# Optimization experiments

Hardware: AMD Instinct MI355X
Metric: run time of the kernel (lower is better)

## Reference

```python
import jax, jax.numpy as jnp
import numpy as np


def setup_inputs() -> dict:
    key = jax.random.key(0)
    k1, k2, k3 = jax.random.split(key, 3)
    N, M, D = 8192, 32768, 64
    source_data = jax.random.normal(k1, (N, D), dtype=jnp.float32)
    target_data = jax.random.normal(k2, (M, D), dtype=jnp.float32)
    psi = jax.random.normal(k3, (M,), dtype=jnp.float32)
    return {"source_data": source_data, "target_data": target_data, "psi": psi}


def reference(source_data, target_data, psi):
    # cost[n, m] = ||x_n||^2 + ||y_m||^2 - 2 <x_n, y_m>
    sq_src = jnp.sum(source_data ** 2, axis=1, keepdims=True)          # [N, 1]
    sq_tgt = jnp.sum(target_data ** 2, axis=1)[None, :]                # [1, M]
    cost = sq_src + sq_tgt - 2.0 * jnp.einsum('nd,md->nm', source_data, target_data)
    out = jnp.min(cost - psi[None, :], axis=1) + jnp.mean(psi)         # [N]
    return out
```

## Files before the change

### kernel.cpp

```cpp
#include <hip/hip_runtime.h>
#include <stdint.h>

typedef float  f32x4v __attribute__((ext_vector_type(4)));
typedef short  s16x8  __attribute__((ext_vector_type(8)));

constexpr int D      = 64;
constexpr int SPLITS = 64;
constexpr int TILE_M = 128;
constexpr int G      = 16;
constexpr int NBUF   = 3;

__device__ __forceinline__ unsigned short f2bf(float f) {
    unsigned int u = __float_as_uint(f);
    u = (u + 0x7FFFu + ((u >> 16) & 1u)) >> 16;
    return (unsigned short)u;
}

__device__ __forceinline__ void gload_lds16(const void* g, void* l) {
    __builtin_amdgcn_global_load_lds((__attribute__((address_space(1))) void*)g,
                                     (__attribute__((address_space(3))) void*)l, 16, 0, 0);
}
__device__ __forceinline__ void gload_lds4(const void* g, void* l) {
    __builtin_amdgcn_global_load_lds((__attribute__((address_space(1))) void*)g,
                                     (__attribute__((address_space(3))) void*)l, 4, 0, 0);
}

__global__ __launch_bounds__(256)
void prep(const float* __restrict__ X, const float* __restrict__ Y,
          const float* __restrict__ psi,
          unsigned short* __restrict__ Xb, unsigned short* __restrict__ Yb,
          float* __restrict__ t, float* __restrict__ sqx,
          float* __restrict__ psum_arr, int N, int M) {
    const int tid  = threadIdx.x;
    const int lane = tid & 63, wave = tid >> 6;
    const int r16  = lane & 15, q = lane >> 4;
    const int NYB = M >> 4, NXB = N >> 4;
    const int b = blockIdx.x;
    __shared__ float red[4];

    if (b < NYB) {
        const int row = b * 16 + wave * 4 + q;
        const float4 v = *reinterpret_cast<const float4*>(Y + (size_t)row * D + r16 * 4);
        uint2 p;
        p.x = (unsigned)f2bf(v.x) | ((unsigned)f2bf(v.y) << 16);
        p.y = (unsigned)f2bf(v.z) | ((unsigned)f2bf(v.w) << 16);
        *reinterpret_cast<uint2*>(Yb + (size_t)row * D + r16 * 4) = p;
        float s = v.x * v.x + v.y * v.y + v.z * v.z + v.w * v.w;
        #pragma unroll
        for (int off = 1; off <= 8; off <<= 1) s += __shfl_xor(s, off);
        if (r16 == 0) t[row] = s - psi[row];
    } else if (b < NYB + NXB) {
        const int row = (b - NYB) * 16 + wave * 4 + q;
        const float4 v = *reinterpret_cast<const float4*>(X + (size_t)row * D + r16 * 4);
        uint2 p;
        p.x = (unsigned)f2bf(-2.f * v.x) | ((unsigned)f2bf(-2.f * v.y) << 16);
        p.y = (unsigned)f2bf(-2.f * v.z) | ((unsigned)f2bf(-2.f * v.w) << 16);
        *reinterpret_cast<uint2*>(Xb + (size_t)row * D + r16 * 4) = p;
        float s = v.x * v.x + v.y * v.y + v.z * v.z + v.w * v.w;
        #pragma unroll
        for (int off = 1; off <= 8; off <<= 1) s += __shfl_xor(s, off);
        if (r16 == 0) sqx[row] = s;
    } else {
        const int g = b - NYB - NXB;
        float s = psi[g * 512 + tid] + psi[g * 512 + 256 + tid];
        #pragma unroll
        for (int off = 1; off <= 32; off <<= 1) s += __shfl_xor(s, off);
        if (lane == 0) red[wave] = s;
        __syncthreads();
        if (tid == 0) psum_arr[g] = red[0] + red[1] + red[2] + red[3];
    }
}

__global__ __launch_bounds__(256, 2)
void sdot_main(const unsigned short* __restrict__ Xb,
               const unsigned short* __restrict__ Yb,
               const float* __restrict__ t,
               float* __restrict__ partial, int M) {
    __shared__ __align__(16) unsigned short ly[NBUF][TILE_M * D];
    __shared__ __align__(16) float lt[NBUF][256];

    const int tid  = threadIdx.x;
    const int wave = tid >> 6, lane = tid & 63;
    const int quad = lane >> 4, r16 = lane & 15;
    const int chunk  = blockIdx.x;
    const int rowgrp = blockIdx.y;
    const int CH      = M / SPLITS;
    const int m_begin = chunk * CH;
    const int NT      = CH / TILE_M;

    s16x8 b[G][2];
    #pragma unroll
    for (int g = 0; g < G; ++g) {
        const int srow = rowgrp * (G * 64) + wave * (G * 16) + g * 16 + r16;
        #pragma unroll
        for (int h = 0; h < 2; ++h)
            b[g][h] = *reinterpret_cast<const s16x8*>(Xb + (size_t)srow * D + h * 32 + quad * 8);
    }

    float rmin[G];
    #pragma unroll
    for (int g = 0; g < G; ++g) rmin[g] = 1e30f;

    auto stage = [&](int buf, int mb) {
        #pragma unroll
        for (int i = 0; i < 4; ++i) {
            const int idx = i * 256 + tid;
            const int row = idx >> 3, c = idx & 7;
            gload_lds16(Yb + (size_t)(mb + row) * D + ((c ^ (row & 7)) << 3),
                        &ly[buf][(i * 256 + wave * 64) << 3]);
        }
        gload_lds4(t + mb + wave * 64 + lane, &lt[buf][wave * 64]);
    };

    stage(0, m_begin);
    stage(1, m_begin + TILE_M);

    for (int tI = 0; tI < NT; ++tI) {
        if (tI < NT - 1) asm volatile("s_waitcnt vmcnt(5)" ::: "memory");
        else             asm volatile("s_waitcnt vmcnt(0)" ::: "memory");
        __builtin_amdgcn_s_barrier();
        if (tI + 2 < NT) stage((tI + 2) % NBUF, m_begin + (tI + 2) * TILE_M);
        const int buf = tI % NBUF;

        #pragma unroll
        for (int st = 0; st < TILE_M / 16; ++st) {
            const int trow = st * 16 + r16;
            const int sw   = trow & 7;
            const s16x8 a0 = *reinterpret_cast<const s16x8*>(
                                 &ly[buf][trow * D + ((quad ^ sw) << 3)]);
            const s16x8 a1 = *reinterpret_cast<const s16x8*>(
                                 &ly[buf][trow * D + (((quad + 4) ^ sw) << 3)]);
            const f32x4v tv4 = *reinterpret_cast<const f32x4v*>(
                                   &lt[buf][st * 16 + quad * 4]);
            #pragma unroll
            for (int g = 0; g < G; ++g) {
                f32x4v acc = __builtin_amdgcn_mfma_f32_16x16x32_bf16(a0, b[g][0], tv4, 0, 0, 0);
                acc        = __builtin_amdgcn_mfma_f32_16x16x32_bf16(a1, b[g][1], acc, 0, 0, 0);
                rmin[g] = fminf(fminf(fminf(acc[0], acc[1]), acc[2]),
                                fminf(acc[3], rmin[g]));
            }
        }
    }

    #pragma unroll
    for (int off = 16; off <= 32; off <<= 1)
        #pragma unroll
        for (int g = 0; g < G; ++g)
            rmin[g] = fminf(rmin[g], __shfl_xor(rmin[g], off));

    if (quad == 0) {
        #pragma unroll
        for (int g = 0; g < G; ++g) {
            const int row = rowgrp * (G * 64) + wave * (G * 16) + g * 16 + r16;
            partial[(size_t)row * SPLITS + chunk] = rmin[g];
        }
    }
}

__global__ __launch_bounds__(256)
void finalize(const float* __restrict__ sqx, const float* __restrict__ partial,
              const float* __restrict__ psum_arr, float* __restrict__ out, int M) {
    const int lane = threadIdx.x & 63, wave = threadIdx.x >> 6;
    const int row  = blockIdx.x * 4 + wave;
    float ps = psum_arr[lane];
    #pragma unroll
    for (int off = 1; off <= 32; off <<= 1) ps += __shfl_xor(ps, off);
    float pm = partial[(size_t)row * SPLITS + lane];
    #pragma unroll
    for (int off = 1; off <= 32; off <<= 1) pm = fminf(pm, __shfl_xor(pm, off));
    if (lane == 0) out[row] = sqx[row] + ps / (float)M + pm;
}

extern "C" void kernel_launch(void* const* d_in, const int* in_sizes, int n_in,
                              void* d_out, int out_size, void* d_ws, size_t ws_size,
                              hipStream_t stream) {
    const float* X   = (const float*)d_in[0];
    const float* Y   = (const float*)d_in[1];
    const float* psi = (const float*)d_in[2];
    float* out = (float*)d_out;

    const int N = in_sizes[0] / D;
    const int M = in_sizes[2];

    char* ws = (char*)d_ws;
    unsigned short* Yb = (unsigned short*)ws;
    size_t off = (size_t)M * D * sizeof(unsigned short);
    unsigned short* Xb = (unsigned short*)(ws + off);
    off += (size_t)N * D * sizeof(unsigned short);
    float* t = (float*)(ws + off);
    off += (size_t)M * sizeof(float);
    float* sqx = (float*)(ws + off);
    off += (size_t)N * sizeof(float);
    float* partial = (float*)(ws + off);
    off += (size_t)N * SPLITS * sizeof(float);
    float* psum_arr = (float*)(ws + off);

    prep<<<(M >> 4) + (N >> 4) + 64, 256, 0, stream>>>(X, Y, psi, Xb, Yb, t, sqx, psum_arr, N, M);
    sdot_main<<<dim3(SPLITS, N / 1024), 256, 0, stream>>>(Xb, Yb, t, partial, M);
    finalize<<<N / 4, 256, 0, stream>>>(sqx, partial, psum_arr, out, M);
}
```

Baseline: 100.6 us.

## Load whole chunk into LDS once and batch MFMAs with raised priority

Replaces the triple-buffered streaming of 128-row target tiles with a single bulk load of the block's full 512-row chunk into LDS, followed by one wait and barrier. The inner loop now issues all 16 first-half MFMAs, then all 16 second-half MFMAs, under s_setprio(1) before doing the min reductions, and hoists the swizzle offsets out of the loop. This removes per-tile barriers and waitcnt stalls and lets independent MFMAs issue back to back. In exchange the initial load latency is fully exposed, LDS use per block grows to about 66 KB, which may limit how many blocks fit per CU, and 16 accumulator vectors raise register pressure.

Result: slower. 105.4 us (+4.8%).

```diff
diff --git a/kernel.cpp b/kernel.cpp
--- a/kernel.cpp
+++ b/kernel.cpp
@@ -6,9 +6,8 @@
 
 constexpr int D      = 64;
 constexpr int SPLITS = 64;
-constexpr int TILE_M = 128;
+constexpr int CHM    = 512;
 constexpr int G      = 16;
-constexpr int NBUF   = 3;
 
 __device__ __forceinline__ unsigned short f2bf(float f) {
     unsigned int u = __float_as_uint(f);
@@ -76,17 +75,26 @@
                const unsigned short* __restrict__ Yb,
                const float* __restrict__ t,
                float* __restrict__ partial, int M) {
-    __shared__ __align__(16) unsigned short ly[NBUF][TILE_M * D];
-    __shared__ __align__(16) float lt[NBUF][256];
+    __shared__ __align__(16) unsigned short ly[CHM * D];
+    __shared__ __align__(16) float lt[CHM];
 
     const int tid  = threadIdx.x;
     const int wave = tid >> 6, lane = tid & 63;
     const int quad = lane >> 4, r16 = lane & 15;
-    const int chunk  = blockIdx.x;
-    const int rowgrp = blockIdx.y;
-    const int CH      = M / SPLITS;
-    const int m_begin = chunk * CH;
-    const int NT      = CH / TILE_M;
+    const int chunk   = blockIdx.x;
+    const int rowgrp  = blockIdx.y;
+    const int m_begin = chunk * CHM;
+
+    #pragma unroll
+    for (int i = 0; i < 16; ++i) {
+        const int idx = i * 256 + tid;
+        const int row = idx >> 3, c = idx & 7;
+        gload_lds16(Yb + (size_t)(m_begin + row) * D + ((c ^ (row & 7)) << 3),
+                    &ly[(i * 256 + wave * 64) << 3]);
+    }
+    #pragma unroll
+    for (int j = 0; j < 2; ++j)
+        gload_lds4(t + m_begin + j * 256 + wave * 64 + lane, &lt[j * 256 + wave * 64]);
 
     s16x8 b[G][2];
     #pragma unroll
@@ -101,45 +109,31 @@
     #pragma unroll
     for (int g = 0; g < G; ++g) rmin[g] = 1e30f;
 
-    auto stage = [&](int buf, int mb) {
+    asm volatile("s_waitcnt vmcnt(0)" ::: "memory");
+    __builtin_amdgcn_s_barrier();
+
+    const int csw0 = (quad ^ (r16 & 7)) << 3;
+    const int csw1 = ((quad + 4) ^ (r16 & 7)) << 3;
+    #pragma unroll 4
+    for (int st = 0; st < CHM / 16; ++st) {
+        const int trow = st * 16 + r16;
+        const s16x8 a0 = *reinterpret_cast<const s16x8*>(&ly[trow * D + csw0]);
+        const s16x8 a1 = *reinterpret_cast<const s16x8*>(&ly[trow * D + csw1]);
+        const f32x4v tv4 = *reinterpret_cast<const f32x4v*>(&lt[st * 16 + quad * 4]);
+
+        f32x4v acc[G];
+        __builtin_amdgcn_s_setprio(1);
         #pragma unroll
-        for (int i = 0; i < 4; ++i) {
-            const int idx = i * 256 + tid;
-            const int row = idx >> 3, c = idx & 7;
-            gload_lds16(Yb + (size_t)(mb + row) * D + ((c ^ (row & 7)) << 3),
-                        &ly[buf][(i * 256 + wave * 64) << 3]);
-        }
-        gload_lds4(t + mb + wave * 64 + lane, &lt[buf][wave * 64]);
-    };
-
-    stage(0, m_begin);
-    stage(1, m_begin + TILE_M);
-
-    for (int tI = 0; tI < NT; ++tI) {
-        if (tI < NT - 1) asm volatile("s_waitcnt vmcnt(5)" ::: "memory");
-        else             asm volatile("s_waitcnt vmcnt(0)" ::: "memory");
-        __builtin_amdgcn_s_barrier();
-        if (tI + 2 < NT) stage((tI + 2) % NBUF, m_begin + (tI + 2) * TILE_M);
-        const int buf = tI % NBUF;
-
+        for (int g = 0; g < G; ++g)
+            acc[g] = __builtin_amdgcn_mfma_f32_16x16x32_bf16(a0, b[g][0], tv4, 0, 0, 0);
         #pragma unroll
-        for (int st = 0; st < TILE_M / 16; ++st) {
-            const int trow = st * 16 + r16;
-            const int sw   = trow & 7;
-            const s16x8 a0 = *reinterpret_cast<const s16x8*>(
-                                 &ly[buf][trow * D + ((quad ^ sw) << 3)]);
-            const s16x8 a1 = *reinterpret_cast<const s16x8*>(
-                                 &ly[buf][trow * D + (((quad + 4) ^ sw) << 3)]);
-            const f32x4v tv4 = *reinterpret_cast<const f32x4v*>(
-                                   &lt[buf][st * 16 + quad * 4]);
-            #pragma unroll
-            for (int g = 0; g < G; ++g) {
-                f32x4v acc = __builtin_amdgcn_mfma_f32_16x16x32_bf16(a0, b[g][0], tv4, 0, 0, 0);
-                acc        = __builtin_amdgcn_mfma_f32_16x16x32_bf16(a1, b[g][1], acc, 0, 0, 0);
-                rmin[g] = fminf(fminf(fminf(acc[0], acc[1]), acc[2]),
-                                fminf(acc[3], rmin[g]));
-            }
-        }
+        for (int g = 0; g < G; ++g)
+            acc[g] = __builtin_amdgcn_mfma_f32_16x16x32_bf16(a1, b[g][1], acc[g], 0, 0, 0);
+        __builtin_amdgcn_s_setprio(0);
+        #pragma unroll
+        for (int g = 0; g < G; ++g)
+            rmin[g] = fminf(fminf(fminf(acc[g][0], acc[g][1]),
+                                  fminf(acc[g][2], acc[g][3])), rmin[g]);
     }
 
     #pragma unroll
@@ -196,6 +190,6 @@
     float* psum_arr = (float*)(ws + off);
 
     prep<<<(M >> 4) + (N >> 4) + 64, 256, 0, stream>>>(X, Y, psi, Xb, Yb, t, sqx, psum_arr, N, M);
-    sdot_main<<<dim3(SPLITS, N / 1024), 256, 0, stream>>>(Xb, Yb, t, partial, M);
+    sdot_main<<<dim3(SPLITS, N / (G * 64)), 256, 0, stream>>>(Xb, Yb, t, partial, M);
     finalize<<<N / 4, 256, 0, stream>>>(sqx, partial, psum_arr, out, M);
 }
```
